# Kernel tuning notes

Measured on AMD Instinct MI355X. Metric: run time of the kernel, lower is better.

Reference implementation:

```python
import jax, jax.numpy as jnp
import numpy as np

EPS = 1e-6
B, N_NEG, H, D = 256, 1000, 3, 128
NUM_CLUSTER = (25000, 2500, 250)
NUM_IMG = 100000

def _l2norm(x):
    # matches torch F.normalize(dim=-1): x / max(||x||, 1e-12)
    n = jnp.sqrt(jnp.sum(x * x, axis=-1, keepdims=True))
    return x / jnp.maximum(n, 1e-12)

def setup_inputs() -> dict:
    key = jax.random.key(0)
    ks = jax.random.split(key, 10)
    return {
        "semantic_embs": jax.random.normal(ks[0], (B, H * D), dtype=jnp.float32),
        "centroids0": jax.random.normal(ks[1], (NUM_CLUSTER[0], D), dtype=jnp.float32),
        "centroids1": jax.random.normal(ks[2], (NUM_CLUSTER[1], D), dtype=jnp.float32),
        "centroids2": jax.random.normal(ks[3], (NUM_CLUSTER[2], D), dtype=jnp.float32),
        "im2cluster0": jax.random.randint(ks[4], (NUM_IMG,), 0, NUM_CLUSTER[0], dtype=jnp.int32),
        "im2cluster1": jax.random.randint(ks[5], (NUM_IMG,), 0, NUM_CLUSTER[1], dtype=jnp.int32),
        "im2cluster2": jax.random.randint(ks[6], (NUM_IMG,), 0, NUM_CLUSTER[2], dtype=jnp.int32),
        "index": jax.random.randint(ks[7], (B,), 0, NUM_IMG, dtype=jnp.int32),
        "neg_im2cluster": jax.random.randint(ks[8], (B, N_NEG, H), 0, min(NUM_CLUSTER), dtype=jnp.int32),
    }

def reference(semantic_embs, centroids0, centroids1, centroids2,
              im2cluster0, im2cluster1, im2cluster2, index, neg_im2cluster):
    cents = [centroids0, centroids1, centroids2]
    i2c = [im2cluster0, im2cluster1, im2cluster2]
    b = semantic_embs.shape[0]
    se = _l2norm(semantic_embs.reshape(b, H, D))                 # [B,H,D]

    # positive path: gather centroid of each sample's cluster per hierarchy
    pos = jnp.stack([_l2norm(cents[h][i2c[h][index]]) for h in range(H)], axis=1)  # [B,H,D]
    pos_path_sim = jnp.prod((jnp.sum(se * pos, axis=-1) + 1.0) * 0.5, axis=1)      # [B]
    pos_loss = -jnp.log(pos_path_sim + EPS)                                        # [B]

    # negative paths: gather sampled centroids per hierarchy
    neg = jnp.stack([_l2norm(cents[h][neg_im2cluster[:, :, h]]) for h in range(H)], axis=2)  # [B,N,H,D]
    neg_proto_sim = jnp.sum(se[:, None, :, :] * neg, axis=-1)                      # [B,N,H]
    neg_path_sim = jnp.prod((neg_proto_sim + 1.0) * 0.5, axis=-1)                  # [B,N]
    neg_loss = -jnp.log(1.0 - neg_path_sim + EPS)                                  # [B,N]

    # true_negative mask: neg path differs from positive path in any hierarchy
    pos_lab = jnp.stack([i2c[h][index] for h in range(H)], axis=-1)                # [B,H]
    tn = jnp.any(neg_im2cluster != pos_lab[:, None, :], axis=-1).astype(se.dtype)  # [B,N]
    neg_loss = jnp.sum(neg_loss * tn, axis=-1) / (jnp.sum(tn, axis=-1) + EPS)      # [B]

    return jnp.mean(jnp.stack([pos_loss, neg_loss], axis=-1))
```

## Files before the change

kernel.cpp:

```cpp
#include <hip/hip_runtime.h>
#include <math.h>

#define EPS   1e-6f
#define BB    256
#define NNEG  1000
#define HH    3
#define DD    128
#define NCN   250

#define OFF_CENT_T   0
#define OFF_SE_N     96000
#define OFF_POS_LOSS 194304
#define OFF_SIM      194560
#define OFF_POS_LAB  386560

__global__ void k1_cent_prep(const float* __restrict__ c0,
                             const float* __restrict__ c1,
                             const float* __restrict__ c2,
                             float* __restrict__ centT) {
    int wid  = blockIdx.x * 4 + (threadIdx.x >> 6);
    int lane = threadIdx.x & 63;
    if (wid >= HH * NCN) return;
    int h = wid / NCN;
    int c = wid - h * NCN;
    const float* cp = (h == 0) ? c0 : (h == 1) ? c1 : c2;
    const float2 v = *(const float2*)(cp + (size_t)c * DD + lane * 2);
    float ss = v.x * v.x + v.y * v.y;
    #pragma unroll
    for (int off = 32; off; off >>= 1) ss += __shfl_xor(ss, off);
    float inv = 1.0f / fmaxf(sqrtf(ss), 1e-12f);
    float* base = centT + h * (DD * NCN);
    base[(lane * 2)     * NCN + c] = v.x * inv;
    base[(lane * 2 + 1) * NCN + c] = v.y * inv;
}

__global__ void k2_se_pos(const float* __restrict__ se,
                          const float* __restrict__ c0,
                          const float* __restrict__ c1,
                          const float* __restrict__ c2,
                          const int* __restrict__ i2c0,
                          const int* __restrict__ i2c1,
                          const int* __restrict__ i2c2,
                          const int* __restrict__ index,
                          float* __restrict__ se_n,
                          float* __restrict__ pos_loss,
                          int* __restrict__ pos_lab) {
    int b    = blockIdx.x;
    int h    = threadIdx.x >> 6;
    int lane = threadIdx.x & 63;
    __shared__ float ph_s[HH];

    const float2 s = *(const float2*)(se + (size_t)b * (HH * DD) + h * DD + lane * 2);
    float ss = s.x * s.x + s.y * s.y;
    #pragma unroll
    for (int off = 32; off; off >>= 1) ss += __shfl_xor(ss, off);
    float inv = 1.0f / fmaxf(sqrtf(ss), 1e-12f);
    float2 sn = make_float2(s.x * inv, s.y * inv);
    float* sp = se_n + ((size_t)b * HH + h) * DD + lane * 2;
    sp[0] = sn.x; sp[1] = sn.y;

    int idx  = index[b];
    const int*   ip = (h == 0) ? i2c0 : (h == 1) ? i2c1 : i2c2;
    const float* cp = (h == 0) ? c0   : (h == 1) ? c1   : c2;
    int cidx = ip[idx];
    const float2 cv = *(const float2*)(cp + (size_t)cidx * DD + lane * 2);
    float dot = sn.x * cv.x + sn.y * cv.y;
    float csq = cv.x * cv.x + cv.y * cv.y;
    #pragma unroll
    for (int off = 32; off; off >>= 1) {
        dot += __shfl_xor(dot, off);
        csq += __shfl_xor(csq, off);
    }
    if (lane == 0) {
        float invc = 1.0f / fmaxf(sqrtf(csq), 1e-12f);
        ph_s[h] = (dot * invc + 1.0f) * 0.5f;
        pos_lab[b * HH + h] = cidx;
    }
    __syncthreads();
    if (threadIdx.x == 0)
        pos_loss[b] = -logf(ph_s[0] * ph_s[1] * ph_s[2] + EPS);
}

__global__ void k3_sim(const float* __restrict__ se_n,
                       const float* __restrict__ centT,
                       float* __restrict__ sim) {
    int b = blockIdx.x, h = blockIdx.y;
    int tid = threadIdx.x;
    __shared__ float sse[DD];
    if (tid < DD) sse[tid] = se_n[((size_t)b * HH + h) * DD + tid];
    __syncthreads();
    if (tid < NCN) {
        const float* ct = centT + h * (DD * NCN) + tid;
        float acc = 0.0f;
        #pragma unroll 8
        for (int d = 0; d < DD; ++d) acc = fmaf(sse[d], ct[d * NCN], acc);
        sim[((size_t)b * HH + h) * NCN + tid] = (acc + 1.0f) * 0.5f;
    }
}

__global__ void k4_neg(const int* __restrict__ negc,
                       const float* __restrict__ sim,
                       const int* __restrict__ pos_lab,
                       const float* __restrict__ pos_loss,
                       float* __restrict__ out) {
    int b = blockIdx.x, tid = threadIdx.x;
    __shared__ float ssim[HH * NCN];
    __shared__ int   slab[HH];
    __shared__ float wL[4], wT[4];
    for (int i = tid; i < HH * NCN; i += 256) ssim[i] = sim[(size_t)b * HH * NCN + i];
    if (tid < HH) slab[tid] = pos_lab[b * HH + tid];
    __syncthreads();
    int l0 = slab[0], l1 = slab[1], l2 = slab[2];
    float accL = 0.0f, accT = 0.0f;
    for (int n = tid; n < NNEG; n += 256) {
        const int* q = negc + ((size_t)b * NNEG + n) * HH;
        int i0 = q[0], i1 = q[1], i2 = q[2];
        float p = ssim[i0] * ssim[NCN + i1] * ssim[2 * NCN + i2];
        if (i0 != l0 || i1 != l1 || i2 != l2) {
            accL -= logf(1.0f - p + EPS);
            accT += 1.0f;
        }
    }
    #pragma unroll
    for (int off = 32; off; off >>= 1) {
        accL += __shfl_xor(accL, off);
        accT += __shfl_xor(accT, off);
    }
    int wid = tid >> 6, lane = tid & 63;
    if (lane == 0) { wL[wid] = accL; wT[wid] = accT; }
    __syncthreads();
    if (tid == 0) {
        float L = wL[0] + wL[1] + wL[2] + wL[3];
        float T = wT[0] + wT[1] + wT[2] + wT[3];
        float nb = L / (T + EPS);
        atomicAdd(out, (pos_loss[b] + nb) * (1.0f / (2.0f * BB)));
    }
}

extern "C" void kernel_launch(void* const* d_in, const int* in_sizes, int n_in,
                              void* d_out, int out_size, void* d_ws, size_t ws_size,
                              hipStream_t stream) {
    const float* se    = (const float*)d_in[0];
    const float* c0    = (const float*)d_in[1];
    const float* c1    = (const float*)d_in[2];
    const float* c2    = (const float*)d_in[3];
    const int*   i2c0  = (const int*)d_in[4];
    const int*   i2c1  = (const int*)d_in[5];
    const int*   i2c2  = (const int*)d_in[6];
    const int*   index = (const int*)d_in[7];
    const int*   negc  = (const int*)d_in[8];

    float* ws       = (float*)d_ws;
    float* centT    = ws + OFF_CENT_T;
    float* se_n     = ws + OFF_SE_N;
    float* pos_loss = ws + OFF_POS_LOSS;
    float* sim      = ws + OFF_SIM;
    int*   pos_lab  = (int*)(ws + OFF_POS_LAB);
    float* out      = (float*)d_out;

    hipMemsetAsync(out, 0, sizeof(float), stream);

    hipLaunchKernelGGL(k1_cent_prep, dim3((HH * NCN + 3) / 4), dim3(256), 0, stream,
                       c0, c1, c2, centT);
    hipLaunchKernelGGL(k2_se_pos, dim3(BB), dim3(192), 0, stream,
                       se, c0, c1, c2, i2c0, i2c1, i2c2, index, se_n, pos_loss, pos_lab);
    hipLaunchKernelGGL(k3_sim, dim3(BB, HH), dim3(256), 0, stream, se_n, centT, sim);
    hipLaunchKernelGGL(k4_neg, dim3(BB), dim3(256), 0, stream,
                       negc, sim, pos_lab, pos_loss, out);
}
```

Baseline: 97.61 us.

## Fuse normalize, similarity and negative-loss kernels into one per-sample kernel

The separate se/pos, similarity and negative-loss kernels are merged into a single per-sample block. Normalized embeddings and the per-sample similarity table now stay in shared memory rather than passing through global workspace. The memset of the output is folded into the prep kernel, so the host issues two launches instead of five operations. The cost is that the similarity matmul now runs with only 256 blocks of 256 threads instead of 768 blocks, so there is less parallelism in that phase.

```diff
diff --git a/kernel.cpp b/kernel.cpp
--- a/kernel.cpp
+++ b/kernel.cpp
@@ -9,19 +9,17 @@
 #define NCN   250
 
 #define OFF_CENT_T   0
-#define OFF_SE_N     96000
-#define OFF_POS_LOSS 194304
-#define OFF_SIM      194560
-#define OFF_POS_LAB  386560
 
-__global__ void k1_cent_prep(const float* __restrict__ c0,
-                             const float* __restrict__ c1,
-                             const float* __restrict__ c2,
-                             float* __restrict__ centT) {
+__global__ void kA_prep(const float* __restrict__ c0,
+                        const float* __restrict__ c1,
+                        const float* __restrict__ c2,
+                        float* __restrict__ centT,
+                        float* __restrict__ out) {
+    if (blockIdx.x == 0 && threadIdx.x == 0) out[0] = 0.0f;
     int wid  = blockIdx.x * 4 + (threadIdx.x >> 6);
     int lane = threadIdx.x & 63;
     if (wid >= HH * NCN) return;
-    int h = wid / NCN;
+    int h = (wid >= 2 * NCN) ? 2 : (wid >= NCN ? 1 : 0);
     int c = wid - h * NCN;
     const float* cp = (h == 0) ? c0 : (h == 1) ? c1 : c2;
     const float2 v = *(const float2*)(cp + (size_t)c * DD + lane * 2);
@@ -34,82 +32,70 @@
     base[(lane * 2 + 1) * NCN + c] = v.y * inv;
 }
 
-__global__ void k2_se_pos(const float* __restrict__ se,
-                          const float* __restrict__ c0,
-                          const float* __restrict__ c1,
-                          const float* __restrict__ c2,
-                          const int* __restrict__ i2c0,
-                          const int* __restrict__ i2c1,
-                          const int* __restrict__ i2c2,
-                          const int* __restrict__ index,
-                          float* __restrict__ se_n,
-                          float* __restrict__ pos_loss,
-                          int* __restrict__ pos_lab) {
-    int b    = blockIdx.x;
-    int h    = threadIdx.x >> 6;
-    int lane = threadIdx.x & 63;
-    __shared__ float ph_s[HH];
+__global__ __launch_bounds__(256) void kB_main(
+        const float* __restrict__ se,
+        const float* __restrict__ c0,
+        const float* __restrict__ c1,
+        const float* __restrict__ c2,
+        const int* __restrict__ i2c0,
+        const int* __restrict__ i2c1,
+        const int* __restrict__ i2c2,
+        const int* __restrict__ index,
+        const int* __restrict__ negc,
+        const float* __restrict__ centT,
+        float* __restrict__ out) {
+    int b = blockIdx.x;
+    int tid = threadIdx.x, wave = tid >> 6, lane = tid & 63;
 
-    const float2 s = *(const float2*)(se + (size_t)b * (HH * DD) + h * DD + lane * 2);
-    float ss = s.x * s.x + s.y * s.y;
-    #pragma unroll
-    for (int off = 32; off; off >>= 1) ss += __shfl_xor(ss, off);
-    float inv = 1.0f / fmaxf(sqrtf(ss), 1e-12f);
-    float2 sn = make_float2(s.x * inv, s.y * inv);
-    float* sp = se_n + ((size_t)b * HH + h) * DD + lane * 2;
-    sp[0] = sn.x; sp[1] = sn.y;
+    __shared__ float sse[HH * DD];
+    __shared__ float ssim[HH * NCN];
+    __shared__ int   slab[HH];
+    __shared__ float ph[HH];
+    __shared__ float wL[4], wT[4];
 
-    int idx  = index[b];
-    const int*   ip = (h == 0) ? i2c0 : (h == 1) ? i2c1 : i2c2;
-    const float* cp = (h == 0) ? c0   : (h == 1) ? c1   : c2;
-    int cidx = ip[idx];
-    const float2 cv = *(const float2*)(cp + (size_t)cidx * DD + lane * 2);
-    float dot = sn.x * cv.x + sn.y * cv.y;
-    float csq = cv.x * cv.x + cv.y * cv.y;
-    #pragma unroll
-    for (int off = 32; off; off >>= 1) {
-        dot += __shfl_xor(dot, off);
-        csq += __shfl_xor(csq, off);
-    }
-    if (lane == 0) {
-        float invc = 1.0f / fmaxf(sqrtf(csq), 1e-12f);
-        ph_s[h] = (dot * invc + 1.0f) * 0.5f;
-        pos_lab[b * HH + h] = cidx;
+    if (wave < HH) {
+        int h = wave;
+        const float2 s = *(const float2*)(se + (size_t)b * (HH * DD) + h * DD + lane * 2);
+        float ss = s.x * s.x + s.y * s.y;
+        #pragma unroll
+        for (int off = 32; off; off >>= 1) ss += __shfl_xor(ss, off);
+        float inv = 1.0f / fmaxf(sqrtf(ss), 1e-12f);
+        float2 sn = make_float2(s.x * inv, s.y * inv);
+        sse[h * DD + lane * 2]     = sn.x;
+        sse[h * DD + lane * 2 + 1] = sn.y;
+
+        int idx = index[b];
+        const int*   ip = (h == 0) ? i2c0 : (h == 1) ? i2c1 : i2c2;
+        const float* cp = (h == 0) ? c0   : (h == 1) ? c1   : c2;
+        int cidx = ip[idx];
+        const float2 cv = *(const float2*)(cp + (size_t)cidx * DD + lane * 2);
+        float dot = sn.x * cv.x + sn.y * cv.y;
+        float csq = cv.x * cv.x + cv.y * cv.y;
+        #pragma unroll
+        for (int off = 32; off; off >>= 1) {
+            dot += __shfl_xor(dot, off);
+            csq += __shfl_xor(csq, off);
+        }
+        if (lane == 0) {
+            float invc = 1.0f / fmaxf(sqrtf(csq), 1e-12f);
+            ph[h]   = (dot * invc + 1.0f) * 0.5f;
+            slab[h] = cidx;
+        }
     }
     __syncthreads();
-    if (threadIdx.x == 0)
-        pos_loss[b] = -logf(ph_s[0] * ph_s[1] * ph_s[2] + EPS);
-}
 
-__global__ void k3_sim(const float* __restrict__ se_n,
-                       const float* __restrict__ centT,
-                       float* __restrict__ sim) {
-    int b = blockIdx.x, h = blockIdx.y;
-    int tid = threadIdx.x;
-    __shared__ float sse[DD];
-    if (tid < DD) sse[tid] = se_n[((size_t)b * HH + h) * DD + tid];
-    __syncthreads();
-    if (tid < NCN) {
-        const float* ct = centT + h * (DD * NCN) + tid;
+    for (int j = tid; j < HH * NCN; j += 256) {
+        int h = (j >= 2 * NCN) ? 2 : (j >= NCN ? 1 : 0);
+        int c = j - h * NCN;
+        const float* ct = centT + h * (DD * NCN) + c;
+        const float* sh = sse + h * DD;
         float acc = 0.0f;
         #pragma unroll 8
-        for (int d = 0; d < DD; ++d) acc = fmaf(sse[d], ct[d * NCN], acc);
-        sim[((size_t)b * HH + h) * NCN + tid] = (acc + 1.0f) * 0.5f;
+        for (int d = 0; d < DD; ++d) acc = fmaf(sh[d], ct[d * NCN], acc);
+        ssim[j] = (acc + 1.0f) * 0.5f;
     }
-}
+    __syncthreads();
 
-__global__ void k4_neg(const int* __restrict__ negc,
-                       const float* __restrict__ sim,
-                       const int* __restrict__ pos_lab,
-                       const float* __restrict__ pos_loss,
-                       float* __restrict__ out) {
-    int b = blockIdx.x, tid = threadIdx.x;
-    __shared__ float ssim[HH * NCN];
-    __shared__ int   slab[HH];
-    __shared__ float wL[4], wT[4];
-    for (int i = tid; i < HH * NCN; i += 256) ssim[i] = sim[(size_t)b * HH * NCN + i];
-    if (tid < HH) slab[tid] = pos_lab[b * HH + tid];
-    __syncthreads();
     int l0 = slab[0], l1 = slab[1], l2 = slab[2];
     float accL = 0.0f, accT = 0.0f;
     for (int n = tid; n < NNEG; n += 256) {
@@ -126,14 +112,15 @@
         accL += __shfl_xor(accL, off);
         accT += __shfl_xor(accT, off);
     }
-    int wid = tid >> 6, lane = tid & 63;
-    if (lane == 0) { wL[wid] = accL; wT[wid] = accT; }
+    if (lane == 0) { wL[wave] = accL; wT[wave] = accT; }
     __syncthreads();
+
     if (tid == 0) {
         float L = wL[0] + wL[1] + wL[2] + wL[3];
         float T = wT[0] + wT[1] + wT[2] + wT[3];
-        float nb = L / (T + EPS);
-        atomicAdd(out, (pos_loss[b] + nb) * (1.0f / (2.0f * BB)));
+        float neg_b = L / (T + EPS);
+        float pos_b = -logf(ph[0] * ph[1] * ph[2] + EPS);
+        atomicAdd(out, (pos_b + neg_b) * (1.0f / (2.0f * BB)));
     }
 }
 
@@ -150,21 +137,11 @@
     const int*   index = (const int*)d_in[7];
     const int*   negc  = (const int*)d_in[8];
 
-    float* ws       = (float*)d_ws;
-    float* centT    = ws + OFF_CENT_T;
-    float* se_n     = ws + OFF_SE_N;
-    float* pos_loss = ws + OFF_POS_LOSS;
-    float* sim      = ws + OFF_SIM;
-    int*   pos_lab  = (int*)(ws + OFF_POS_LAB);
-    float* out      = (float*)d_out;
+    float* centT = (float*)d_ws + OFF_CENT_T;
+    float* out   = (float*)d_out;
 
-    hipMemsetAsync(out, 0, sizeof(float), stream);
-
-    hipLaunchKernelGGL(k1_cent_prep, dim3((HH * NCN + 3) / 4), dim3(256), 0, stream,
-                       c0, c1, c2, centT);
-    hipLaunchKernelGGL(k2_se_pos, dim3(BB), dim3(192), 0, stream,
-                       se, c0, c1, c2, i2c0, i2c1, i2c2, index, se_n, pos_loss, pos_lab);
-    hipLaunchKernelGGL(k3_sim, dim3(BB, HH), dim3(256), 0, stream, se_n, centT, sim);
-    hipLaunchKernelGGL(k4_neg, dim3(BB), dim3(256), 0, stream,
-                       negc, sim, pos_lab, pos_loss, out);
+    hipLaunchKernelGGL(kA_prep, dim3((HH * NCN + 3) / 4), dim3(256), 0, stream,
+                       c0, c1, c2, centT, out);
+    hipLaunchKernelGGL(kB_main, dim3(BB), dim3(256), 0, stream,
+                       se, c0, c1, c2, i2c0, i2c1, i2c2, index, negc, centT, out);
 }
```

Measured after the change: 100.4 us. +2.8%, slower.
